# Kernel optimization log

Hardware: AMD Instinct MI355X
Metric: run time of the kernel (lower is better)

Reference implementation:

```python
import jax, jax.numpy as jnp
import numpy as np
import math

D_MODEL = 512
NUM_HEADS = 8
B, S = 2, 4096


def setup_inputs() -> dict:
    key = jax.random.key(0)
    ks = jax.random.split(key, 11)
    d = D_MODEL
    sc = 1.0 / math.sqrt(d)
    return {
        "query": jax.random.normal(ks[0], (B, S, d), jnp.float32),
        "key": jax.random.normal(ks[1], (B, S, d), jnp.float32),
        "value": jax.random.normal(ks[2], (B, S, d), jnp.float32),
        "Wq": jax.random.normal(ks[3], (d, d), jnp.float32) * sc,
        "bq": jnp.zeros((d,), jnp.float32),
        "Wk": jax.random.normal(ks[4], (d, d), jnp.float32) * sc,
        "bk": jnp.zeros((d,), jnp.float32),
        "Wv": jax.random.normal(ks[5], (d, d), jnp.float32) * sc,
        "bv": jnp.zeros((d,), jnp.float32),
        "Wo": jax.random.normal(ks[6], (d, d), jnp.float32) * sc,
        "bo": jnp.zeros((d,), jnp.float32),
    }


def reference(query, key, value, Wq, bq, Wk, bk, Wv, bv, Wo, bo):
    b, q_len, d_model = query.shape
    k_len = key.shape[1]
    h = NUM_HEADS
    d_k = d_model // h
    q = (query @ Wq.T + bq).reshape(b, q_len, h, d_k)
    k = (key @ Wk.T + bk).reshape(b, k_len, h, d_k)
    v = (value @ Wv.T + bv).reshape(b, k_len, h, d_k)
    # NOTE: faithful to source — softmax WITHOUT pre-scaling, then divide by sqrt(d_k)
    comp = jnp.einsum('bqhd,bkhd->bhqk', q, k)
    attn = jax.nn.softmax(comp, axis=-1) / jnp.sqrt(jnp.asarray(d_k, comp.dtype))
    x = jnp.einsum('bhqk,bkhd->bqhd', attn, v)
    return x.reshape(b, q_len, d_model) @ Wo.T + bo
```

## Files before the change

kernel.cpp:

```cpp
#include <hip/hip_runtime.h>

typedef _Float16 f16;
typedef __fp16 fp16x2 __attribute__((ext_vector_type(2)));
typedef _Float16 half4 __attribute__((ext_vector_type(4)));
typedef _Float16 half8 __attribute__((ext_vector_type(8)));
typedef float f32x4 __attribute__((ext_vector_type(4)));
typedef float float4v __attribute__((ext_vector_type(4)));

#define LOG2E 1.44269504088896340736f

__device__ __forceinline__ half8 cat8(half4 a, half4 b) {
    half8 r;
    r[0] = a[0]; r[1] = a[1]; r[2] = a[2]; r[3] = a[3];
    r[4] = b[0]; r[5] = b[1]; r[6] = b[2]; r[7] = b[3];
    return r;
}

union H8 { fp16x2 h2[4]; half8 h8; };

#define TR8(baddr, d0,d1,d2,d3,d4,d5,d6,d7)                                   \
  asm volatile("ds_read_b64_tr_b16 %0, %8 offset:0\n\t"                       \
               "ds_read_b64_tr_b16 %1, %8 offset:512\n\t"                     \
               "ds_read_b64_tr_b16 %2, %8 offset:128\n\t"                     \
               "ds_read_b64_tr_b16 %3, %8 offset:640\n\t"                     \
               "ds_read_b64_tr_b16 %4, %8 offset:256\n\t"                     \
               "ds_read_b64_tr_b16 %5, %8 offset:768\n\t"                     \
               "ds_read_b64_tr_b16 %6, %8 offset:384\n\t"                     \
               "ds_read_b64_tr_b16 %7, %8 offset:896"                         \
               : "=v"(d0),"=v"(d1),"=v"(d2),"=v"(d3),                         \
                 "=v"(d4),"=v"(d5),"=v"(d6),"=v"(d7)                          \
               : "v"(baddr) : "memory")

#define LGKM0_FENCE()                                                          \
  do { asm volatile("s_waitcnt lgkmcnt(0)" ::: "memory");                      \
       __builtin_amdgcn_sched_barrier(0); } while (0)

__global__ __launch_bounds__(256) void qkv_proj(
    const float* __restrict__ Aq, const float* __restrict__ Ak, const float* __restrict__ Av,
    const float* __restrict__ Wq, const float* __restrict__ Wk, const float* __restrict__ Wv,
    const float* __restrict__ bq, const float* __restrict__ bk, const float* __restrict__ bv,
    f16* __restrict__ Qh, f16* __restrict__ Kh, f16* __restrict__ Vh)
{
    const int z = blockIdx.z;
    const float* __restrict__ A    = (z == 0) ? Aq : (z == 1) ? Ak : Av;
    const float* __restrict__ W    = (z == 0) ? Wq : (z == 1) ? Wk : Wv;
    const float* __restrict__ bias = (z == 0) ? bq : (z == 1) ? bk : bv;
    f16* __restrict__ dst          = (z == 0) ? Qh : (z == 1) ? Kh : Vh;

    __shared__ __align__(16) f16 As[128 * 40];
    __shared__ __align__(16) f16 Ws[128 * 40];

    const int t  = threadIdx.x;
    const int m0 = blockIdx.y * 128;
    const int n0 = blockIdx.x * 128;
    const int w = t >> 6, lane = t & 63, lr = lane & 15, lg = lane >> 4;
    const int wr = w >> 1, wc = w & 1;

    f32x4 acc[4][4] = {};

    for (int k0 = 0; k0 < 512; k0 += 32) {
        #pragma unroll
        for (int it = 0; it < 2; ++it) {
            int c = t + it * 256;
            int row  = c >> 2;
            int col8 = (c & 3) * 8;

            const float* ga = A + (size_t)(m0 + row) * 512 + k0 + col8;
            float4v a0 = *(const float4v*)ga;
            float4v a1 = *(const float4v*)(ga + 4);
            half8 ha;
            ha[0] = (f16)a0[0]; ha[1] = (f16)a0[1]; ha[2] = (f16)a0[2]; ha[3] = (f16)a0[3];
            ha[4] = (f16)a1[0]; ha[5] = (f16)a1[1]; ha[6] = (f16)a1[2]; ha[7] = (f16)a1[3];
            *(half8*)&As[row * 40 + col8] = ha;

            const float* gw = W + (size_t)(n0 + row) * 512 + k0 + col8;
            float4v w0 = *(const float4v*)gw;
            float4v w1 = *(const float4v*)(gw + 4);
            half8 hw;
            hw[0] = (f16)w0[0]; hw[1] = (f16)w0[1]; hw[2] = (f16)w0[2]; hw[3] = (f16)w0[3];
            hw[4] = (f16)w1[0]; hw[5] = (f16)w1[1]; hw[6] = (f16)w1[2]; hw[7] = (f16)w1[3];
            *(half8*)&Ws[row * 40 + col8] = hw;
        }
        __syncthreads();

        half8 af[4], bf[4];
        #pragma unroll
        for (int i = 0; i < 4; ++i) {
            af[i] = *(const half8*)&As[(wr * 64 + i * 16 + lr) * 40 + lg * 8];
            bf[i] = *(const half8*)&Ws[(wc * 64 + i * 16 + lr) * 40 + lg * 8];
        }
        #pragma unroll
        for (int mi = 0; mi < 4; ++mi)
            #pragma unroll
            for (int ni = 0; ni < 4; ++ni)
                acc[mi][ni] = __builtin_amdgcn_mfma_f32_16x16x32_f16(af[mi], bf[ni], acc[mi][ni], 0, 0, 0);
        __syncthreads();
    }

    #pragma unroll
    for (int mi = 0; mi < 4; ++mi) {
        #pragma unroll
        for (int ni = 0; ni < 4; ++ni) {
            int col = n0 + wc * 64 + ni * 16 + lr;
            float bv_ = bias[col];
            int h  = col >> 6;
            int dd = col & 63;
            #pragma unroll
            for (int r = 0; r < 4; ++r) {
                int row = m0 + wr * 64 + mi * 16 + lg * 4 + r;
                int b = row >> 12;
                int s = row & 4095;
                dst[(((size_t)(b * 8 + h)) * 4096 + s) * 64 + dd] = (f16)(acc[mi][ni][r] + bv_);
            }
        }
    }
}

__global__ __launch_bounds__(512, 4) void flash_attn(
    const f16* __restrict__ Qh, const f16* __restrict__ Kh, const f16* __restrict__ Vh,
    f16* __restrict__ Xh)
{
    const int bh  = blockIdx.y;
    const int t = threadIdx.x, w = t >> 6, lane = t & 63, lr = lane & 15, lg = lane >> 4;
    const int q0 = blockIdx.x * 128 + w * 16;

    __shared__ __align__(16) f16 Ks[2][64 * 72];
    __shared__ __align__(16) f16 Vs[2][64 * 64];

    const size_t hb = (size_t)bh * (4096 * 64);

    half8 aq0 = *(const half8*)&Qh[hb + (size_t)(q0 + lr) * 64 + lg * 8];
    half8 aq1 = *(const half8*)&Qh[hb + (size_t)(q0 + lr) * 64 + 32 + lg * 8];

    const int srow = t >> 3;
    const int scol = (t & 7) * 8;
    const int kdst = srow * 72 + scol;
    const int vdst = ((((srow >> 2) & 3) * 16) + (srow >> 4) * 4 + (scol >> 4)) * 64
                   + (srow & 3) * 16 + (scol & 15);

    f32x4 o[4] = {};
    float mL = -INFINITY, l = 0.0f;

    half8 kreg = *(const half8*)&Kh[hb + (size_t)srow * 64 + scol];
    half8 vreg = *(const half8*)&Vh[hb + (size_t)srow * 64 + scol];

    for (int kt = 0; kt < 4096; kt += 64) {
        const int bi = (kt >> 6) & 1;
        f16* ks = &Ks[bi][0];
        f16* vs = &Vs[bi][0];

        *(half8*)&ks[kdst] = kreg;
        *(half8*)&vs[vdst] = vreg;
        __syncthreads();

        int ktn = (kt + 64) & 4095;
        kreg = *(const half8*)&Kh[hb + (size_t)(ktn + srow) * 64 + scol];
        vreg = *(const half8*)&Vh[hb + (size_t)(ktn + srow) * 64 + scol];

        f32x4 sf[4] = {};
        #pragma unroll
        for (int c = 0; c < 2; ++c) {
            half8 kf[4];
            #pragma unroll
            for (int kb = 0; kb < 4; ++kb)
                kf[kb] = *(const half8*)&ks[(kb * 16 + lr) * 72 + c * 32 + lg * 8];
            half8 aqc = c ? aq1 : aq0;
            __builtin_amdgcn_s_setprio(1);
            #pragma unroll
            for (int kb = 0; kb < 4; ++kb)
                sf[kb] = __builtin_amdgcn_mfma_f32_16x16x32_f16(kf[kb], aqc, sf[kb], 0, 0, 0);
            __builtin_amdgcn_s_setprio(0);
        }

        float vm01 = fmaxf(fmaxf(fmaxf(sf[0][0], sf[0][1]), fmaxf(sf[0][2], sf[0][3])),
                           fmaxf(fmaxf(sf[1][0], sf[1][1]), fmaxf(sf[1][2], sf[1][3])));
        float vm23 = fmaxf(fmaxf(fmaxf(sf[2][0], sf[2][1]), fmaxf(sf[2][2], sf[2][3])),
                           fmaxf(fmaxf(sf[3][0], sf[3][1]), fmaxf(sf[3][2], sf[3][3])));
        float vm = fmaxf(vm01, vm23);
        vm = fmaxf(vm, __shfl_xor(vm, 16, 64));
        vm = fmaxf(vm, __shfl_xor(vm, 32, 64));
        float vmL = vm * LOG2E;

        if (__any(vmL > mL + 8.0f)) {
            float mn = fmaxf(mL, vmL);
            float al = __builtin_amdgcn_exp2f(mL - mn);
            l *= al;
            #pragma unroll
            for (int db = 0; db < 4; ++db) o[db] *= al;
            mL = mn;
        }

        f32x4 pe[4];
        float rs = 0.0f;
        #pragma unroll
        for (int kb = 0; kb < 4; ++kb) {
            #pragma unroll
            for (int ro = 0; ro < 4; ++ro) {
                float p = __builtin_amdgcn_exp2f(fmaf(sf[kb][ro], LOG2E, -mL));
                pe[kb][ro] = p;
                rs += p;
            }
        }
        rs += __shfl_xor(rs, 16, 64);
        rs += __shfl_xor(rs, 32, 64);
        l += rs;

        H8 pb0u, pb1u;
        pb0u.h2[0] = __builtin_amdgcn_cvt_pkrtz(pe[0][0], pe[0][1]);
        pb0u.h2[1] = __builtin_amdgcn_cvt_pkrtz(pe[0][2], pe[0][3]);
        pb0u.h2[2] = __builtin_amdgcn_cvt_pkrtz(pe[1][0], pe[1][1]);
        pb0u.h2[3] = __builtin_amdgcn_cvt_pkrtz(pe[1][2], pe[1][3]);
        pb1u.h2[0] = __builtin_amdgcn_cvt_pkrtz(pe[2][0], pe[2][1]);
        pb1u.h2[1] = __builtin_amdgcn_cvt_pkrtz(pe[2][2], pe[2][3]);
        pb1u.h2[2] = __builtin_amdgcn_cvt_pkrtz(pe[3][0], pe[3][1]);
        pb1u.h2[3] = __builtin_amdgcn_cvt_pkrtz(pe[3][2], pe[3][3]);

        const unsigned vb = (unsigned)(size_t)vs + (unsigned)(lg * 2048 + lr * 8);
        {
            half4 u0,u1,u2,u3,u4,u5,u6,u7;
            TR8(vb, u0,u1,u2,u3,u4,u5,u6,u7);
            LGKM0_FENCE();
            __builtin_amdgcn_s_setprio(1);
            o[0] = __builtin_amdgcn_mfma_f32_16x16x32_f16(cat8(u0,u1), pb0u.h8, o[0], 0, 0, 0);
            o[1] = __builtin_amdgcn_mfma_f32_16x16x32_f16(cat8(u2,u3), pb0u.h8, o[1], 0, 0, 0);
            o[2] = __builtin_amdgcn_mfma_f32_16x16x32_f16(cat8(u4,u5), pb0u.h8, o[2], 0, 0, 0);
            o[3] = __builtin_amdgcn_mfma_f32_16x16x32_f16(cat8(u6,u7), pb0u.h8, o[3], 0, 0, 0);
            __builtin_amdgcn_s_setprio(0);
            TR8(vb + 1024u, u0,u1,u2,u3,u4,u5,u6,u7);
            LGKM0_FENCE();
            __builtin_amdgcn_s_setprio(1);
            o[0] = __builtin_amdgcn_mfma_f32_16x16x32_f16(cat8(u0,u1), pb1u.h8, o[0], 0, 0, 0);
            o[1] = __builtin_amdgcn_mfma_f32_16x16x32_f16(cat8(u2,u3), pb1u.h8, o[1], 0, 0, 0);
            o[2] = __builtin_amdgcn_mfma_f32_16x16x32_f16(cat8(u4,u5), pb1u.h8, o[2], 0, 0, 0);
            o[3] = __builtin_amdgcn_mfma_f32_16x16x32_f16(cat8(u6,u7), pb1u.h8, o[3], 0, 0, 0);
            __builtin_amdgcn_s_setprio(0);
        }
    }

    const int b = bh >> 3, h = bh & 7;
    const float inv = 1.0f / (l * 8.0f);
    const int q = q0 + lr;
    #pragma unroll
    for (int db = 0; db < 4; ++db) {
        half4 hv;
        hv[0] = (f16)(o[db][0] * inv);
        hv[1] = (f16)(o[db][1] * inv);
        hv[2] = (f16)(o[db][2] * inv);
        hv[3] = (f16)(o[db][3] * inv);
        *(half4*)&Xh[((size_t)(b * 4096 + q)) * 512 + h * 64 + db * 16 + lg * 4] = hv;
    }
}

__global__ __launch_bounds__(256) void out_proj(
    const f16* __restrict__ Xh, const float* __restrict__ Wo, const float* __restrict__ bo,
    float* __restrict__ out)
{
    __shared__ __align__(16) f16 As[128 * 40];
    __shared__ __align__(16) f16 Ws[128 * 40];

    const int t  = threadIdx.x;
    const int m0 = blockIdx.y * 128;
    const int n0 = blockIdx.x * 128;
    const int w = t >> 6, lane = t & 63, lr = lane & 15, lg = lane >> 4;
    const int wr = w >> 1, wc = w & 1;

    f32x4 acc[4][4] = {};

    for (int k0 = 0; k0 < 512; k0 += 32) {
        #pragma unroll
        for (int it = 0; it < 2; ++it) {
            int c = t + it * 256;
            int row  = c >> 2;
            int col8 = (c & 3) * 8;

            *(half8*)&As[row * 40 + col8] =
                *(const half8*)&Xh[(size_t)(m0 + row) * 512 + k0 + col8];

            const float* gw = Wo + (size_t)(n0 + row) * 512 + k0 + col8;
            float4v w0 = *(const float4v*)gw;
            float4v w1 = *(const float4v*)(gw + 4);
            half8 hw;
            hw[0] = (f16)w0[0]; hw[1] = (f16)w0[1]; hw[2] = (f16)w0[2]; hw[3] = (f16)w0[3];
            hw[4] = (f16)w1[0]; hw[5] = (f16)w1[1]; hw[6] = (f16)w1[2]; hw[7] = (f16)w1[3];
            *(half8*)&Ws[row * 40 + col8] = hw;
        }
        __syncthreads();

        half8 af[4], bf[4];
        #pragma unroll
        for (int i = 0; i < 4; ++i) {
            af[i] = *(const half8*)&As[(wr * 64 + i * 16 + lr) * 40 + lg * 8];
            bf[i] = *(const half8*)&Ws[(wc * 64 + i * 16 + lr) * 40 + lg * 8];
        }
        #pragma unroll
        for (int mi = 0; mi < 4; ++mi)
            #pragma unroll
            for (int ni = 0; ni < 4; ++ni)
                acc[mi][ni] = __builtin_amdgcn_mfma_f32_16x16x32_f16(af[mi], bf[ni], acc[mi][ni], 0, 0, 0);
        __syncthreads();
    }

    #pragma unroll
    for (int mi = 0; mi < 4; ++mi) {
        #pragma unroll
        for (int ni = 0; ni < 4; ++ni) {
            int col = n0 + wc * 64 + ni * 16 + lr;
            float bb = bo[col];
            #pragma unroll
            for (int r = 0; r < 4; ++r) {
                int row = m0 + wr * 64 + mi * 16 + lg * 4 + r;
                out[(size_t)row * 512 + col] = acc[mi][ni][r] + bb;
            }
        }
    }
}

extern "C" void kernel_launch(void* const* d_in, const int* in_sizes, int n_in,
                              void* d_out, int out_size, void* d_ws, size_t ws_size,
                              hipStream_t stream) {
    const float* query = (const float*)d_in[0];
    const float* key   = (const float*)d_in[1];
    const float* value = (const float*)d_in[2];
    const float* Wq    = (const float*)d_in[3];
    const float* bq    = (const float*)d_in[4];
    const float* Wk    = (const float*)d_in[5];
    const float* bk    = (const float*)d_in[6];
    const float* Wv    = (const float*)d_in[7];
    const float* bv    = (const float*)d_in[8];
    const float* Wo    = (const float*)d_in[9];
    const float* bo    = (const float*)d_in[10];
    float* out = (float*)d_out;

    char* ws = (char*)d_ws;
    f16* Qh = (f16*)(ws);
    f16* Kh = (f16*)(ws + 8388608);
    f16* Vh = (f16*)(ws + 16777216);
    f16* Xh = (f16*)(ws + 25165824);

    qkv_proj<<<dim3(4, 64, 3), 256, 0, stream>>>(query, key, value,
                                                 Wq, Wk, Wv, bq, bk, bv,
                                                 Qh, Kh, Vh);
    flash_attn<<<dim3(32, 16), 512, 0, stream>>>(Qh, Kh, Vh, Xh);
    out_proj<<<dim3(4, 64), 256, 0, stream>>>(Xh, Wo, bo, out);
}
```

Before: 174.1 us.

## Process two 16-row query tiles per wave in flash attention

Each wave now handles 32 query rows as two independent 16-row tiles, so every K fragment and transposed V read from LDS feeds twice as many MFMAs. The grid is halved to 256 blocks, with launch bounds relaxed to 2 blocks per CU to allow more registers. This amortises LDS traffic and the K/V global loads per query row. The cost is more register pressure and fewer blocks: 256 blocks on a GPU with 256 CUs gives about one block per CU, which may reduce latency hiding.

```diff
diff --git a/kernel.cpp b/kernel.cpp
--- a/kernel.cpp
+++ b/kernel.cpp
@@ -27,13 +27,59 @@
                "ds_read_b64_tr_b16 %5, %8 offset:768\n\t"                     \
                "ds_read_b64_tr_b16 %6, %8 offset:384\n\t"                     \
                "ds_read_b64_tr_b16 %7, %8 offset:896"                         \
-               : "=v"(d0),"=v"(d1),"=v"(d2),"=v"(d3),                         \
-                 "=v"(d4),"=v"(d5),"=v"(d6),"=v"(d7)                          \
+               : "=&v"(d0),"=&v"(d1),"=&v"(d2),"=&v"(d3),                     \
+                 "=&v"(d4),"=&v"(d5),"=&v"(d6),"=&v"(d7)                      \
                : "v"(baddr) : "memory")
 
 #define LGKM0_FENCE()                                                          \
   do { asm volatile("s_waitcnt lgkmcnt(0)" ::: "memory");                      \
        __builtin_amdgcn_sched_barrier(0); } while (0)
+
+__device__ __forceinline__ void softmax_pack(
+    f32x4 sf[4], float& mL, float& l, f32x4 o[4], H8& pb0, H8& pb1)
+{
+    float vm01 = fmaxf(fmaxf(fmaxf(sf[0][0], sf[0][1]), fmaxf(sf[0][2], sf[0][3])),
+                       fmaxf(fmaxf(sf[1][0], sf[1][1]), fmaxf(sf[1][2], sf[1][3])));
+    float vm23 = fmaxf(fmaxf(fmaxf(sf[2][0], sf[2][1]), fmaxf(sf[2][2], sf[2][3])),
+                       fmaxf(fmaxf(sf[3][0], sf[3][1]), fmaxf(sf[3][2], sf[3][3])));
+    float vm = fmaxf(vm01, vm23);
+    vm = fmaxf(vm, __shfl_xor(vm, 16, 64));
+    vm = fmaxf(vm, __shfl_xor(vm, 32, 64));
+    float vmL = vm * LOG2E;
+
+    if (__any(vmL > mL + 8.0f)) {
+        float mn = fmaxf(mL, vmL);
+        float al = __builtin_amdgcn_exp2f(mL - mn);
+        l *= al;
+        #pragma unroll
+        for (int db = 0; db < 4; ++db) o[db] *= al;
+        mL = mn;
+    }
+
+    f32x4 pe[4];
+    float rs = 0.0f;
+    #pragma unroll
+    for (int kb = 0; kb < 4; ++kb) {
+        #pragma unroll
+        for (int ro = 0; ro < 4; ++ro) {
+            float p = __builtin_amdgcn_exp2f(fmaf(sf[kb][ro], LOG2E, -mL));
+            pe[kb][ro] = p;
+            rs += p;
+        }
+    }
+    rs += __shfl_xor(rs, 16, 64);
+    rs += __shfl_xor(rs, 32, 64);
+    l += rs;
+
+    pb0.h2[0] = __builtin_amdgcn_cvt_pkrtz(pe[0][0], pe[0][1]);
+    pb0.h2[1] = __builtin_amdgcn_cvt_pkrtz(pe[0][2], pe[0][3]);
+    pb0.h2[2] = __builtin_amdgcn_cvt_pkrtz(pe[1][0], pe[1][1]);
+    pb0.h2[3] = __builtin_amdgcn_cvt_pkrtz(pe[1][2], pe[1][3]);
+    pb1.h2[0] = __builtin_amdgcn_cvt_pkrtz(pe[2][0], pe[2][1]);
+    pb1.h2[1] = __builtin_amdgcn_cvt_pkrtz(pe[2][2], pe[2][3]);
+    pb1.h2[2] = __builtin_amdgcn_cvt_pkrtz(pe[3][0], pe[3][1]);
+    pb1.h2[3] = __builtin_amdgcn_cvt_pkrtz(pe[3][2], pe[3][3]);
+}
 
 __global__ __launch_bounds__(256) void qkv_proj(
     const float* __restrict__ Aq, const float* __restrict__ Ak, const float* __restrict__ Av,
@@ -116,21 +162,23 @@
     }
 }
 
-__global__ __launch_bounds__(512, 4) void flash_attn(
+__global__ __launch_bounds__(512, 2) void flash_attn(
     const f16* __restrict__ Qh, const f16* __restrict__ Kh, const f16* __restrict__ Vh,
     f16* __restrict__ Xh)
 {
     const int bh  = blockIdx.y;
     const int t = threadIdx.x, w = t >> 6, lane = t & 63, lr = lane & 15, lg = lane >> 4;
-    const int q0 = blockIdx.x * 128 + w * 16;
+    const int q0 = blockIdx.x * 256 + w * 32;
 
     __shared__ __align__(16) f16 Ks[2][64 * 72];
     __shared__ __align__(16) f16 Vs[2][64 * 64];
 
     const size_t hb = (size_t)bh * (4096 * 64);
 
-    half8 aq0 = *(const half8*)&Qh[hb + (size_t)(q0 + lr) * 64 + lg * 8];
-    half8 aq1 = *(const half8*)&Qh[hb + (size_t)(q0 + lr) * 64 + 32 + lg * 8];
+    half8 aq00 = *(const half8*)&Qh[hb + (size_t)(q0 + lr) * 64 + lg * 8];
+    half8 aq01 = *(const half8*)&Qh[hb + (size_t)(q0 + lr) * 64 + 32 + lg * 8];
+    half8 aq10 = *(const half8*)&Qh[hb + (size_t)(q0 + 16 + lr) * 64 + lg * 8];
+    half8 aq11 = *(const half8*)&Qh[hb + (size_t)(q0 + 16 + lr) * 64 + 32 + lg * 8];
 
     const int srow = t >> 3;
     const int scol = (t & 7) * 8;
@@ -138,11 +186,14 @@
     const int vdst = ((((srow >> 2) & 3) * 16) + (srow >> 4) * 4 + (scol >> 4)) * 64
                    + (srow & 3) * 16 + (scol & 15);
 
-    f32x4 o[4] = {};
-    float mL = -INFINITY, l = 0.0f;
-
-    half8 kreg = *(const half8*)&Kh[hb + (size_t)srow * 64 + scol];
-    half8 vreg = *(const half8*)&Vh[hb + (size_t)srow * 64 + scol];
+    f32x4 o0[4] = {}, o1[4] = {};
+    float mL0 = -INFINITY, l0 = 0.0f, mL1 = -INFINITY, l1 = 0.0f;
+
+    const f16* kbase = Kh + hb + (size_t)srow * 64 + scol;
+    const f16* vbase = Vh + hb + (size_t)srow * 64 + scol;
+
+    half8 kreg = *(const half8*)kbase;
+    half8 vreg = *(const half8*)vbase;
 
     for (int kt = 0; kt < 4096; kt += 64) {
         const int bi = (kt >> 6) & 1;
@@ -153,67 +204,32 @@
         *(half8*)&vs[vdst] = vreg;
         __syncthreads();
 
-        int ktn = (kt + 64) & 4095;
-        kreg = *(const half8*)&Kh[hb + (size_t)(ktn + srow) * 64 + scol];
-        vreg = *(const half8*)&Vh[hb + (size_t)(ktn + srow) * 64 + scol];
-
-        f32x4 sf[4] = {};
+        int koff = ((kt + 64) & 4095) << 6;
+        kreg = *(const half8*)(kbase + koff);
+        vreg = *(const half8*)(vbase + koff);
+
+        f32x4 sf0[4] = {}, sf1[4] = {};
         #pragma unroll
         for (int c = 0; c < 2; ++c) {
             half8 kf[4];
             #pragma unroll
             for (int kb = 0; kb < 4; ++kb)
                 kf[kb] = *(const half8*)&ks[(kb * 16 + lr) * 72 + c * 32 + lg * 8];
-            half8 aqc = c ? aq1 : aq0;
+            half8 a0 = c ? aq01 : aq00;
+            half8 a1 = c ? aq11 : aq10;
             __builtin_amdgcn_s_setprio(1);
             #pragma unroll
             for (int kb = 0; kb < 4; ++kb)
-                sf[kb] = __builtin_amdgcn_mfma_f32_16x16x32_f16(kf[kb], aqc, sf[kb], 0, 0, 0);
+                sf0[kb] = __builtin_amdgcn_mfma_f32_16x16x32_f16(kf[kb], a0, sf0[kb], 0, 0, 0);
+            #pragma unroll
+            for (int kb = 0; kb < 4; ++kb)
+                sf1[kb] = __builtin_amdgcn_mfma_f32_16x16x32_f16(kf[kb], a1, sf1[kb], 0, 0, 0);
             __builtin_amdgcn_s_setprio(0);
         }
 
-        float vm01 = fmaxf(fmaxf(fmaxf(sf[0][0], sf[0][1]), fmaxf(sf[0][2], sf[0][3])),
-                           fmaxf(fmaxf(sf[1][0], sf[1][1]), fmaxf(sf[1][2], sf[1][3])));
-        float vm23 = fmaxf(fmaxf(fmaxf(sf[2][0], sf[2][1]), fmaxf(sf[2][2], sf[2][3])),
-                           fmaxf(fmaxf(sf[3][0], sf[3][1]), fmaxf(sf[3][2], sf[3][3])));
-        float vm = fmaxf(vm01, vm23);
-        vm = fmaxf(vm, __shfl_xor(vm, 16, 64));
-        vm = fmaxf(vm, __shfl_xor(vm, 32, 64));
-        float vmL = vm * LOG2E;
-
-        if (__any(vmL > mL + 8.0f)) {
-            float mn = fmaxf(mL, vmL);
-            float al = __builtin_amdgcn_exp2f(mL - mn);
-            l *= al;
-            #pragma unroll
-            for (int db = 0; db < 4; ++db) o[db] *= al;
-            mL = mn;
-        }
-
-        f32x4 pe[4];
-        float rs = 0.0f;
-        #pragma unroll
-        for (int kb = 0; kb < 4; ++kb) {
-            #pragma unroll
-            for (int ro = 0; ro < 4; ++ro) {
-                float p = __builtin_amdgcn_exp2f(fmaf(sf[kb][ro], LOG2E, -mL));
-                pe[kb][ro] = p;
-                rs += p;
-            }
-        }
-        rs += __shfl_xor(rs, 16, 64);
-        rs += __shfl_xor(rs, 32, 64);
-        l += rs;
-
-        H8 pb0u, pb1u;
-        pb0u.h2[0] = __builtin_amdgcn_cvt_pkrtz(pe[0][0], pe[0][1]);
-        pb0u.h2[1] = __builtin_amdgcn_cvt_pkrtz(pe[0][2], pe[0][3]);
-        pb0u.h2[2] = __builtin_amdgcn_cvt_pkrtz(pe[1][0], pe[1][1]);
-        pb0u.h2[3] = __builtin_amdgcn_cvt_pkrtz(pe[1][2], pe[1][3]);
-        pb1u.h2[0] = __builtin_amdgcn_cvt_pkrtz(pe[2][0], pe[2][1]);
-        pb1u.h2[1] = __builtin_amdgcn_cvt_pkrtz(pe[2][2], pe[2][3]);
-        pb1u.h2[2] = __builtin_amdgcn_cvt_pkrtz(pe[3][0], pe[3][1]);
-        pb1u.h2[3] = __builtin_amdgcn_cvt_pkrtz(pe[3][2], pe[3][3]);
+        H8 p00, p01, p10, p11;
+        softmax_pack(sf0, mL0, l0, o0, p00, p01);
+        softmax_pack(sf1, mL1, l1, o1, p10, p11);
 
         const unsigned vb = (unsigned)(size_t)vs + (unsigned)(lg * 2048 + lr * 8);
         {
@@ -221,33 +237,47 @@
             TR8(vb, u0,u1,u2,u3,u4,u5,u6,u7);
             LGKM0_FENCE();
             __builtin_amdgcn_s_setprio(1);
-            o[0] = __builtin_amdgcn_mfma_f32_16x16x32_f16(cat8(u0,u1), pb0u.h8, o[0], 0, 0, 0);
-            o[1] = __builtin_amdgcn_mfma_f32_16x16x32_f16(cat8(u2,u3), pb0u.h8, o[1], 0, 0, 0);
-            o[2] = __builtin_amdgcn_mfma_f32_16x16x32_f16(cat8(u4,u5), pb0u.h8, o[2], 0, 0, 0);
-            o[3] = __builtin_amdgcn_mfma_f32_16x16x32_f16(cat8(u6,u7), pb0u.h8, o[3], 0, 0, 0);
+            o0[0] = __builtin_amdgcn_mfma_f32_16x16x32_f16(cat8(u0,u1), p00.h8, o0[0], 0, 0, 0);
+            o0[1] = __builtin_amdgcn_mfma_f32_16x16x32_f16(cat8(u2,u3), p00.h8, o0[1], 0, 0, 0);
+            o0[2] = __builtin_amdgcn_mfma_f32_16x16x32_f16(cat8(u4,u5), p00.h8, o0[2], 0, 0, 0);
+            o0[3] = __builtin_amdgcn_mfma_f32_16x16x32_f16(cat8(u6,u7), p00.h8, o0[3], 0, 0, 0);
+            o1[0] = __builtin_amdgcn_mfma_f32_16x16x32_f16(cat8(u0,u1), p10.h8, o1[0], 0, 0, 0);
+            o1[1] = __builtin_amdgcn_mfma_f32_16x16x32_f16(cat8(u2,u3), p10.h8, o1[1], 0, 0, 0);
+            o1[2] = __builtin_amdgcn_mfma_f32_16x16x32_f16(cat8(u4,u5), p10.h8, o1[2], 0, 0, 0);
+            o1[3] = __builtin_amdgcn_mfma_f32_16x16x32_f16(cat8(u6,u7), p10.h8, o1[3], 0, 0, 0);
             __builtin_amdgcn_s_setprio(0);
             TR8(vb + 1024u, u0,u1,u2,u3,u4,u5,u6,u7);
             LGKM0_FENCE();
             __builtin_amdgcn_s_setprio(1);
-            o[0] = __builtin_amdgcn_mfma_f32_16x16x32_f16(cat8(u0,u1), pb1u.h8, o[0], 0, 0, 0);
-            o[1] = __builtin_amdgcn_mfma_f32_16x16x32_f16(cat8(u2,u3), pb1u.h8, o[1], 0, 0, 0);
-            o[2] = __builtin_amdgcn_mfma_f32_16x16x32_f16(cat8(u4,u5), pb1u.h8, o[2], 0, 0, 0);
-            o[3] = __builtin_amdgcn_mfma_f32_16x16x32_f16(cat8(u6,u7), pb1u.h8, o[3], 0, 0, 0);
+            o0[0] = __builtin_amdgcn_mfma_f32_16x16x32_f16(cat8(u0,u1), p01.h8, o0[0], 0, 0, 0);
+            o0[1] = __builtin_amdgcn_mfma_f32_16x16x32_f16(cat8(u2,u3), p01.h8, o0[1], 0, 0, 0);
+            o0[2] = __builtin_amdgcn_mfma_f32_16x16x32_f16(cat8(u4,u5), p01.h8, o0[2], 0, 0, 0);
+            o0[3] = __builtin_amdgcn_mfma_f32_16x16x32_f16(cat8(u6,u7), p01.h8, o0[3], 0, 0, 0);
+            o1[0] = __builtin_amdgcn_mfma_f32_16x16x32_f16(cat8(u0,u1), p11.h8, o1[0], 0, 0, 0);
+            o1[1] = __builtin_amdgcn_mfma_f32_16x16x32_f16(cat8(u2,u3), p11.h8, o1[1], 0, 0, 0);
+            o1[2] = __builtin_amdgcn_mfma_f32_16x16x32_f16(cat8(u4,u5), p11.h8, o1[2], 0, 0, 0);
+            o1[3] = __builtin_amdgcn_mfma_f32_16x16x32_f16(cat8(u6,u7), p11.h8, o1[3], 0, 0, 0);
             __builtin_amdgcn_s_setprio(0);
         }
     }
 
     const int b = bh >> 3, h = bh & 7;
-    const float inv = 1.0f / (l * 8.0f);
-    const int q = q0 + lr;
+    const float inv0 = 1.0f / (l0 * 8.0f);
+    const float inv1 = 1.0f / (l1 * 8.0f);
+    const int q0_ = q0 + lr, q1_ = q0 + 16 + lr;
     #pragma unroll
     for (int db = 0; db < 4; ++db) {
-        half4 hv;
-        hv[0] = (f16)(o[db][0] * inv);
-        hv[1] = (f16)(o[db][1] * inv);
-        hv[2] = (f16)(o[db][2] * inv);
-        hv[3] = (f16)(o[db][3] * inv);
-        *(half4*)&Xh[((size_t)(b * 4096 + q)) * 512 + h * 64 + db * 16 + lg * 4] = hv;
+        half4 hv0, hv1;
+        hv0[0] = (f16)(o0[db][0] * inv0);
+        hv0[1] = (f16)(o0[db][1] * inv0);
+        hv0[2] = (f16)(o0[db][2] * inv0);
+        hv0[3] = (f16)(o0[db][3] * inv0);
+        *(half4*)&Xh[((size_t)(b * 4096 + q0_)) * 512 + h * 64 + db * 16 + lg * 4] = hv0;
+        hv1[0] = (f16)(o1[db][0] * inv1);
+        hv1[1] = (f16)(o1[db][1] * inv1);
+        hv1[2] = (f16)(o1[db][2] * inv1);
+        hv1[3] = (f16)(o1[db][3] * inv1);
+        *(half4*)&Xh[((size_t)(b * 4096 + q1_)) * 512 + h * 64 + db * 16 + lg * 4] = hv1;
     }
 }
 
@@ -340,6 +370,6 @@
     qkv_proj<<<dim3(4, 64, 3), 256, 0, stream>>>(query, key, value,
                                                  Wq, Wk, Wv, bq, bk, bv,
                                                  Qh, Kh, Vh);
-    flash_attn<<<dim3(32, 16), 512, 0, stream>>>(Qh, Kh, Vh, Xh);
+    flash_attn<<<dim3(16, 16), 512, 0, stream>>>(Qh, Kh, Vh, Xh);
     out_proj<<<dim3(4, 64), 256, 0, stream>>>(Xh, Wo, bo, out);
 }
```

Measured after the change: 166.3 us. -4.5%, faster.
